# Performance work log

Hardware: AMD Instinct MI355X
Metric: run time of the kernel (lower is better)

## Reference

```python
import jax, jax.numpy as jnp
import numpy as np

B, S, H = 8, 256, 128
LA, LR = 2, 2
L = LA + LR
HD = H // L  # head_size = 32
SCALE = 1.0 / np.sqrt(HD).astype(np.float32)


def setup_inputs() -> dict:
    key = jax.random.key(0)
    ks = jax.random.split(key, 16)
    w = 0.02
    return {
        'hidden_states': jax.random.normal(ks[0], (B, S, H), jnp.float32),
        'attention_mask': jnp.zeros((B, 1, S, S), jnp.float32),
        'abs0': jax.random.normal(ks[1], (B, S, H), jnp.float32),
        'abs1': jax.random.normal(ks[2], (B, S, H), jnp.float32),
        'rel0': jax.random.normal(ks[3], (B, S, S, H), jnp.float32),
        'rel1': jax.random.normal(ks[4], (B, S, S, H), jnp.float32),
        'Wq': jax.random.normal(ks[5], (H, H), jnp.float32) * w,
        'bq': jnp.zeros((H,), jnp.float32),
        'Wk': jax.random.normal(ks[6], (H, H), jnp.float32) * w,
        'bk': jnp.zeros((H,), jnp.float32),
        'Wv': jax.random.normal(ks[7], (H, H), jnp.float32) * w,
        'bv': jnp.zeros((H,), jnp.float32),
        'Wo': jax.random.normal(ks[8], (H, H), jnp.float32) * w,
        'bo': jnp.zeros((H,), jnp.float32),
    }


def reference(hidden_states, attention_mask, abs0, abs1, rel0, rel1,
              Wq, bq, Wk, bk, Wv, bv, Wo, bo):
    # Projections; heads dim is L (= La+Lr), head size HD
    Q = (hidden_states @ Wq + bq).reshape(B, S, L, HD).transpose(0, 2, 1, 3)  # [B,L,S,HD]
    K = (hidden_states @ Wk + bk).reshape(B, S, L, HD).transpose(0, 2, 1, 3)
    V = (hidden_states @ Wv + bv).reshape(B, S, L, HD).transpose(0, 2, 1, 3)

    scores = jnp.einsum('blqh,blkh->blqk', Q, K) * SCALE  # [B,L,S,S]

    # Absolute-kernel heads 0..La-1: key-project only head i's slice of Wk
    for i, ae in enumerate((abs0, abs1)):
        aK = ae @ Wk[:, i * HD:(i + 1) * HD] + bk[i * HD:(i + 1) * HD]  # [B,S,HD]
        scores = scores.at[:, i].add(jnp.einsum('bqh,bkh->bqk', Q[:, i], aK) * SCALE)

    # Relative-kernel heads La..L-1: per-(q,k) relative key slice
    for i, re in enumerate((rel0, rel1)):
        h = LA + i
        rK = re @ Wk[:, h * HD:(h + 1) * HD] + bk[h * HD:(h + 1) * HD]  # [B,S,S,HD]
        scores = scores.at[:, h].add(jnp.einsum('bqh,bqkh->bqk', Q[:, h], rK) * SCALE)

    scores = scores + attention_mask
    probs = jax.nn.softmax(scores, axis=-1)  # [B,L,S,S]

    ctx = jnp.einsum('blqk,blkh->blqh', probs, V)  # [B,L,S,HD]

    for i, ae in enumerate((abs0, abs1)):
        aV = ae @ Wv[:, i * HD:(i + 1) * HD] + bv[i * HD:(i + 1) * HD]  # [B,S,HD]
        ctx = ctx.at[:, i].add(jnp.einsum('bqk,bkh->bqh', probs[:, i], aV))

    for i, re in enumerate((rel0, rel1)):
        h = LA + i
        rV = re @ Wv[:, h * HD:(h + 1) * HD] + bv[h * HD:(h + 1) * HD]  # [B,S,S,HD]
        ctx = ctx.at[:, h].add(jnp.einsum('bqk,bqkh->bqh', probs[:, h], rV))

    ctx = ctx.transpose(0, 2, 1, 3).reshape(B, S, H)
    return ctx @ Wo + bo
```

## Files before the change

### kernel.cpp

```cpp
#include <hip/hip_runtime.h>

#define Bc 8
#define Sc 256
#define Hc 128
#define HDc 32
#define NHc 4
#define SCALE 0.17677669529663687f

__global__ __launch_bounds__(256) void mmha_kernel(
    const float* __restrict__ hs,
    const float* __restrict__ am,
    const float* __restrict__ abs0,
    const float* __restrict__ abs1,
    const float* __restrict__ rel0,
    const float* __restrict__ rel1,
    const float* __restrict__ Wq, const float* __restrict__ bq,
    const float* __restrict__ Wk, const float* __restrict__ bk,
    const float* __restrict__ Wv, const float* __restrict__ bv,
    const float* __restrict__ Wo, const float* __restrict__ bo,
    float* __restrict__ out)
{
    const int t = threadIdx.x;
    const int bqi = blockIdx.x;
    const int b = bqi >> 8;
    const int q = bqi & 255;

    __shared__ float hsrow[Hc];
    __shared__ float Qrow[Hc];
    __shared__ float qk_sh[NHc * Hc];
    __shared__ float cb_sh[NHc];
    __shared__ float mask_row[Sc];
    __shared__ float4 red4[256];
    __shared__ float l_sh[8];
    __shared__ float rbarn[Hc];
    __shared__ float ctx_sh[Hc];

    const size_t rowbase = (size_t)(b * Sc + q) * Hc;

    if (t < Hc) hsrow[t] = hs[rowbase + t];
    mask_row[t] = am[((size_t)(b * Sc) + q) * Sc + t];
    __syncthreads();

    if (t < Hc) {
        float acc = bq[t];
        #pragma unroll 16
        for (int c = 0; c < Hc; ++c) acc += hsrow[c] * Wq[c * Hc + t];
        Qrow[t] = acc;
    }
    __syncthreads();

    if (t < Hc) {
        float pv = Qrow[t] * bk[t];
        #pragma unroll
        for (int off = 16; off >= 1; off >>= 1) pv += __shfl_xor(pv, off, 32);
        if ((t & 31) == 0) cb_sh[t >> 5] = 2.0f * pv;
    }
    for (int rep = 0; rep < 2; ++rep) {
        int idx = rep * 256 + t;
        int h = idx >> 7, cp = idx & 127;
        const float4* wkr = (const float4*)(Wk + cp * Hc + h * HDc);
        const float4* qr  = (const float4*)(Qrow + h * HDc);
        float acc = 0.f;
        #pragma unroll
        for (int j = 0; j < HDc / 4; ++j) {
            float4 wv = wkr[j];
            float4 qv = qr[j];
            acc += wv.x * qv.x + wv.y * qv.y + wv.z * qv.z + wv.w * qv.w;
        }
        qk_sh[h * Hc + cp] = acc;
    }
    __syncthreads();

    const int c4 = t & 31;
    const int part = t >> 5;
    const float4* hs4 = (const float4*)(hs + (size_t)b * Sc * Hc);

    for (int h = 0; h < NHc; ++h) {
        const float* eb;
        if (h == 0)      eb = abs0 + (size_t)b * Sc * Hc;
        else if (h == 1) eb = abs1 + (size_t)b * Sc * Hc;
        else if (h == 2) eb = rel0 + (size_t)(b * Sc + q) * Sc * Hc;
        else             eb = rel1 + (size_t)(b * Sc + q) * Sc * Hc;
        const float4* e4 = (const float4*)eb;

        const float4 qreg = ((const float4*)(qk_sh + h * Hc))[c4];
        const float cb = cb_sh[h];

        float4 acc; acc.x = acc.y = acc.z = acc.w = 0.f;
        float l = 0.f;

        #pragma unroll 4
        for (int r = 0; r < 32; ++r) {
            const int row = r * 8 + part;
            const size_t off = (size_t)row * (Hc / 4) + c4;
            const float4 a = hs4[off];
            const float4 e = e4[off];
            float4 v;
            v.x = a.x + e.x; v.y = a.y + e.y;
            v.z = a.z + e.z; v.w = a.w + e.w;
            float pv = v.x * qreg.x + v.y * qreg.y + v.z * qreg.z + v.w * qreg.w;
            #pragma unroll
            for (int off2 = 16; off2 >= 1; off2 >>= 1) pv += __shfl_xor(pv, off2, 32);
            const float p = __expf((pv + cb) * SCALE + mask_row[row]);
            l += p;
            acc.x += p * v.x; acc.y += p * v.y;
            acc.z += p * v.z; acc.w += p * v.w;
        }

        red4[t] = acc;
        if (c4 == 0) l_sh[part] = l;
        __syncthreads();
        if (t < 32) {
            float4 tot; tot.x = tot.y = tot.z = tot.w = 0.f;
            #pragma unroll
            for (int g = 0; g < 8; ++g) {
                float4 v = red4[g * 32 + t];
                tot.x += v.x; tot.y += v.y; tot.z += v.z; tot.w += v.w;
            }
            float lt = 0.f;
            #pragma unroll
            for (int g = 0; g < 8; ++g) lt += l_sh[g];
            const float inv = 1.0f / lt;
            float4 r; r.x = tot.x * inv; r.y = tot.y * inv;
                      r.z = tot.z * inv; r.w = tot.w * inv;
            ((float4*)rbarn)[t] = r;
        }
        __syncthreads();
        if (t < 32) {
            float cv = 2.0f * bv[h * HDc + t];
            #pragma unroll 8
            for (int c = 0; c < Hc; ++c) cv += rbarn[c] * Wv[c * Hc + h * HDc + t];
            ctx_sh[h * HDc + t] = cv;
        }
        __syncthreads();
    }

    if (t < Hc) {
        float ov = bo[t];
        #pragma unroll 16
        for (int c = 0; c < Hc; ++c) ov += ctx_sh[c] * Wo[c * Hc + t];
        out[rowbase + t] = ov;
    }
}

extern "C" void kernel_launch(void* const* d_in, const int* in_sizes, int n_in,
                              void* d_out, int out_size, void* d_ws, size_t ws_size,
                              hipStream_t stream) {
    const float* hs = (const float*)d_in[0];
    const float* am = (const float*)d_in[1];
    const float* a0 = (const float*)d_in[2];
    const float* a1 = (const float*)d_in[3];
    const float* r0 = (const float*)d_in[4];
    const float* r1 = (const float*)d_in[5];
    const float* Wq = (const float*)d_in[6];
    const float* bq = (const float*)d_in[7];
    const float* Wk = (const float*)d_in[8];
    const float* bk = (const float*)d_in[9];
    const float* Wv = (const float*)d_in[10];
    const float* bv = (const float*)d_in[11];
    const float* Wo = (const float*)d_in[12];
    const float* bo = (const float*)d_in[13];

    mmha_kernel<<<dim3(Bc * Sc), dim3(256), 0, stream>>>(
        hs, am, a0, a1, r0, r1, Wq, bq, Wk, bk, Wv, bv, Wo, bo, (float*)d_out);
}
```

Before: 613.0 us.

## Double-buffer embedding chunks into LDS with async global-to-LDS loads

The per-row embedding tiles (abs/rel) are now streamed in 32-row chunks into a double-buffered LDS area using global_load_lds DMA. The load of the next chunk is issued while the current chunk is being consumed, and the hidden-state rows for each chunk are loaded into registers up front. The goal is to hide global memory latency in the memory-bound streaming loop. In exchange it adds a block barrier per chunk and 32KB of LDS per block, which may lower occupancy.

After: 666.0 us. +8.6%, slower.

```diff
diff --git a/kernel.cpp b/kernel.cpp
--- a/kernel.cpp
+++ b/kernel.cpp
@@ -6,6 +6,13 @@
 #define HDc 32
 #define NHc 4
 #define SCALE 0.17677669529663687f
+#define CROWS 32
+#define NCH (Sc / CROWS)
+#define NFC (NHc * NCH)
+#define CBYTES (CROWS * Hc * 4)
+
+#define GLB(p) ((const __attribute__((address_space(1))) void*)(p))
+#define LDS(p) ((__attribute__((address_space(3))) void*)(p))
 
 __global__ __launch_bounds__(256) void mmha_kernel(
     const float* __restrict__ hs,
@@ -24,7 +31,12 @@
     const int bqi = blockIdx.x;
     const int b = bqi >> 8;
     const int q = bqi & 255;
-
+    const int lane = t & 63;
+    const int wv = t >> 6;
+    const int c4 = t & 31;
+    const int part = t >> 5;
+
+    __shared__ __align__(16) float ebuf[2][CROWS * Hc];
     __shared__ float hsrow[Hc];
     __shared__ float Qrow[Hc];
     __shared__ float qk_sh[NHc * Hc];
@@ -36,6 +48,8 @@
     __shared__ float ctx_sh[Hc];
 
     const size_t rowbase = (size_t)(b * Sc + q) * Hc;
+    const size_t bsh  = (size_t)b * Sc * Hc;
+    const size_t bqsh = (size_t)(b * Sc + q) * Sc * Hc;
 
     if (t < Hc) hsrow[t] = hs[rowbase + t];
     mask_row[t] = am[((size_t)(b * Sc) + q) * Sc + t];
@@ -63,48 +77,72 @@
         float acc = 0.f;
         #pragma unroll
         for (int j = 0; j < HDc / 4; ++j) {
-            float4 wv = wkr[j];
+            float4 wvv = wkr[j];
             float4 qv = qr[j];
-            acc += wv.x * qv.x + wv.y * qv.y + wv.z * qv.z + wv.w * qv.w;
+            acc += wvv.x * qv.x + wvv.y * qv.y + wvv.z * qv.z + wvv.w * qv.w;
         }
         qk_sh[h * Hc + cp] = acc;
     }
     __syncthreads();
 
-    const int c4 = t & 31;
-    const int part = t >> 5;
-    const float4* hs4 = (const float4*)(hs + (size_t)b * Sc * Hc);
+    const float* e_abs0 = abs0 + bsh;
+    const float* e_abs1 = abs1 + bsh;
+    const float* e_rel0 = rel0 + bqsh;
+    const float* e_rel1 = rel1 + bqsh;
+
+    auto cbase = [&](int fc) -> const char* {
+        const int hh = fc >> 3;
+        const float* base = (hh == 0) ? e_abs0 : (hh == 1) ? e_abs1
+                          : (hh == 2) ? e_rel0 : e_rel1;
+        return (const char*)base + (size_t)(fc & 7) * CBYTES;
+    };
+    auto dma = [&](int fc) {
+        const char* g = cbase(fc);
+        float* lb = ebuf[fc & 1];
+        #pragma unroll
+        for (int i = 0; i < 4; ++i) {
+            const int s = wv * 4 + i;
+            __builtin_amdgcn_global_load_lds(GLB(g + s * 1024 + lane * 16),
+                                             LDS(lb + s * 256), 16, 0, 0);
+        }
+    };
+
+    dma(0);
+    const float4* hs4 = (const float4*)(hs + bsh);
 
     for (int h = 0; h < NHc; ++h) {
-        const float* eb;
-        if (h == 0)      eb = abs0 + (size_t)b * Sc * Hc;
-        else if (h == 1) eb = abs1 + (size_t)b * Sc * Hc;
-        else if (h == 2) eb = rel0 + (size_t)(b * Sc + q) * Sc * Hc;
-        else             eb = rel1 + (size_t)(b * Sc + q) * Sc * Hc;
-        const float4* e4 = (const float4*)eb;
-
         const float4 qreg = ((const float4*)(qk_sh + h * Hc))[c4];
         const float cb = cb_sh[h];
-
         float4 acc; acc.x = acc.y = acc.z = acc.w = 0.f;
         float l = 0.f;
 
-        #pragma unroll 4
-        for (int r = 0; r < 32; ++r) {
-            const int row = r * 8 + part;
-            const size_t off = (size_t)row * (Hc / 4) + c4;
-            const float4 a = hs4[off];
-            const float4 e = e4[off];
-            float4 v;
-            v.x = a.x + e.x; v.y = a.y + e.y;
-            v.z = a.z + e.z; v.w = a.w + e.w;
-            float pv = v.x * qreg.x + v.y * qreg.y + v.z * qreg.z + v.w * qreg.w;
+        for (int cc = 0; cc < NCH; ++cc) {
+            const int fc = h * NCH + cc;
+            __syncthreads();
+            const int k0 = cc * CROWS;
+            float4 a0 = hs4[(size_t)(k0 +      part) * (Hc / 4) + c4];
+            float4 a1 = hs4[(size_t)(k0 +  8 + part) * (Hc / 4) + c4];
+            float4 a2 = hs4[(size_t)(k0 + 16 + part) * (Hc / 4) + c4];
+            float4 a3 = hs4[(size_t)(k0 + 24 + part) * (Hc / 4) + c4];
+            if (fc + 1 < NFC) dma(fc + 1);
+
+            const float4* eb4 = (const float4*)ebuf[fc & 1];
             #pragma unroll
-            for (int off2 = 16; off2 >= 1; off2 >>= 1) pv += __shfl_xor(pv, off2, 32);
-            const float p = __expf((pv + cb) * SCALE + mask_row[row]);
-            l += p;
-            acc.x += p * v.x; acc.y += p * v.y;
-            acc.z += p * v.z; acc.w += p * v.w;
+            for (int j = 0; j < 4; ++j) {
+                const int lr = j * 8 + part;
+                const float4 a = (j == 0) ? a0 : (j == 1) ? a1 : (j == 2) ? a2 : a3;
+                const float4 e = eb4[lr * (Hc / 4) + c4];
+                float4 v;
+                v.x = a.x + e.x; v.y = a.y + e.y;
+                v.z = a.z + e.z; v.w = a.w + e.w;
+                float pv = v.x * qreg.x + v.y * qreg.y + v.z * qreg.z + v.w * qreg.w;
+                #pragma unroll
+                for (int off2 = 16; off2 >= 1; off2 >>= 1) pv += __shfl_xor(pv, off2, 32);
+                const float p = __expf((pv + cb) * SCALE + mask_row[k0 + lr]);
+                l += p;
+                acc.x += p * v.x; acc.y += p * v.y;
+                acc.z += p * v.z; acc.w += p * v.w;
+            }
         }
 
         red4[t] = acc;
```
